# Optimization experiments

Hardware: AMD Instinct MI355X
Metric: run time of the kernel (lower is better)

## Reference

```python
import jax, jax.numpy as jnp
import numpy as np


def setup_inputs() -> dict:
    key = jax.random.key(0)
    k1, k2, k3, k4 = jax.random.split(key, 4)
    batch, n_channels, t = 4, 2048, 2048
    n_blocks, block_size, ks = 128, 64, 16
    n_block_row = n_channels // block_size  # 32
    x = jax.random.normal(k1, (batch, n_channels, t), dtype=jnp.float32)
    block_values = jax.random.normal(k2, (n_blocks, block_size, block_size, ks), dtype=jnp.float32) * 0.05
    cols = jax.random.randint(k3, (n_blocks,), 0, n_block_row, dtype=jnp.int32)
    rows = jax.random.randint(k4, (n_blocks,), 0, n_block_row, dtype=jnp.int32)
    return {"x": x, "block_values": block_values, "cols": cols, "rows": rows}


def reference(x, block_values, cols, rows):
    # x: (B, C, T); block_values: (n_blocks, bs, bs, ks)
    batch, n_channels, t = x.shape
    n_blocks, bs, _, ks = block_values.shape
    n_block_row = -(-n_channels // bs)
    pad = n_block_row * bs - n_channels
    if pad > 0:
        x = jnp.pad(x, ((0, 0), (0, pad), (0, 0)))
    xb = x.reshape(batch, n_block_row, bs, t)
    # gather active block rows: (B, n_blocks, bs, T) -> (B, n_blocks*bs, T)
    x_unfold = xb[:, cols].reshape(batch, n_blocks * bs, t)
    # grouped causal conv: weights shared across batch, groups = n_blocks
    W = block_values.reshape(n_blocks * bs, bs, ks)  # (O, I/g, K)
    o = jax.lax.conv_general_dilated(
        x_unfold, W,
        window_strides=(1,),
        padding=[(ks - 1, 0)],  # causal: equals padding=ks-1 then [..., :t]
        dimension_numbers=("NCH", "OIH", "NCH"),
        feature_group_count=n_blocks,
    )  # (B, n_blocks*bs, T)
    o = o.reshape(batch, n_blocks, bs, t)
    # scatter-add block outputs into their target block rows
    y = jnp.zeros((batch, n_block_row, bs, t), o.dtype).at[:, rows].add(o)
    y = y.reshape(batch, n_block_row * bs, t)
    return y[:, :n_channels, :]
```

## Files before the change

### kernel.cpp

```cpp
#include <hip/hip_runtime.h>
#include <hip/hip_bf16.h>
#include <stdint.h>

typedef __bf16 bf16_t;
typedef bf16_t bf16x8 __attribute__((ext_vector_type(8)));
typedef float f32x4 __attribute__((ext_vector_type(4)));

#define T_LEN 2048
#define C_LEN 2048
#define NB 128
#define TN 256
#define SROWS 2064
#define XROWS 288

#define GLL(gp, lp) __builtin_amdgcn_global_load_lds( \
    (const __attribute__((address_space(1))) uint32_t*)(gp), \
    (__attribute__((address_space(3))) uint32_t*)(lp), 16, 0, 0)

__global__ __launch_bounds__(256) void prepack_kernel(
    const float* __restrict__ bv, bf16_t* __restrict__ wpk)
{
  const int blk = blockIdx.x;
  const int mt  = blockIdx.y;
  const int tid = threadIdx.x;
  __shared__ float lw[16 * 64 * 17];

  const float* src = bv + (size_t)blk * 65536 + (size_t)mt * 16384;
  for (int p = 0; p < 16; ++p) {
    int idx = p * 1024 + tid * 4;
    const float4 v = *(const float4*)(src + idx);
    int o = idx >> 10;
    int i = (idx >> 4) & 63;
    int k = idx & 15;
    float* d = &lw[(o * 64 + i) * 17 + k];
    d[0] = v.x; d[1] = v.y; d[2] = v.z; d[3] = v.w;
  }
  __syncthreads();

  const int e0 = tid * 2;
  const int l  = e0 >> 3;
  const int j  = e0 & 7;
  const int o  = l & 15;
  for (int ks = 0; ks < 32; ++ks) {
    const int k  = ks >> 1;
    const int i0 = (ks & 1) * 32 + (l >> 4) * 8 + j;
    const float a = lw[(o * 64 + i0) * 17 + k];
    const float b = lw[(o * 64 + i0 + 1) * 17 + k];
    const uint16_t ba = __builtin_bit_cast(uint16_t, (bf16_t)a);
    const uint16_t bb = __builtin_bit_cast(uint16_t, (bf16_t)b);
    const uint32_t packed = (uint32_t)ba | ((uint32_t)bb << 16);
    const size_t off = ((((size_t)blk * 32 + ks) * 4 + mt) * 512) + e0;
    *(uint32_t*)(wpk + off) = packed;
  }
}

__global__ __launch_bounds__(256) void padzero_kernel(bf16_t* __restrict__ S)
{
  const int p = blockIdx.x;
  const size_t g = (p < 64) ? ((size_t)(p >> 4) * SROWS + (p & 15))
                            : ((size_t)4 * SROWS + (p - 64));
  uint4 z = {0u, 0u, 0u, 0u};
  *(uint4*)(S + g * C_LEN + (size_t)threadIdx.x * 8) = z;
}

__global__ __launch_bounds__(256) void xprep_kernel(
    const float* __restrict__ x, bf16_t* __restrict__ S)
{
  const int tb = blockIdx.x, cb = blockIdx.y, n = blockIdx.z;
  const int tid = threadIdx.x;
  __shared__ float lt[64 * 67 + 4];

  #pragma unroll
  for (int p = 0; p < 4; ++p) {
    const int idx = p * 256 + tid;
    const int c   = idx >> 4;
    const int t4  = (idx & 15) * 4;
    const float4 v = *(const float4*)(
        x + ((size_t)n * C_LEN + cb * 64 + c) * T_LEN + tb * 64 + t4);
    float* d = &lt[c * 67 + t4];
    d[0] = v.x; d[1] = v.y; d[2] = v.z; d[3] = v.w;
  }
  __syncthreads();

  #pragma unroll
  for (int p = 0; p < 2; ++p) {
    const int idx = p * 256 + tid;
    const int tl  = idx >> 3;
    const int seg = idx & 7;
    const int t   = tb * 64 + tl;
    const int cbase = (seg * 8) ^ ((t & 7) << 3);
    uint32_t w[4];
    #pragma unroll
    for (int h = 0; h < 4; ++h) {
      const float a = lt[(cbase + 2 * h) * 67 + tl];
      const float b = lt[(cbase + 2 * h + 1) * 67 + tl];
      const uint16_t ba = __builtin_bit_cast(uint16_t, (bf16_t)a);
      const uint16_t bb = __builtin_bit_cast(uint16_t, (bf16_t)b);
      w[h] = (uint32_t)ba | ((uint32_t)bb << 16);
    }
    uint4 u4 = {w[0], w[1], w[2], w[3]};
    *(uint4*)(S + ((size_t)n * SROWS + 16 + t) * C_LEN + cb * 64 + seg * 8) = u4;
  }
}

__global__ __launch_bounds__(256, 2) void bsconv_kernel(
    const bf16_t* __restrict__ S, const bf16_t* __restrict__ wpk,
    const int* __restrict__ cols, const int* __restrict__ rows,
    float* __restrict__ y)
{
  const int tt = blockIdx.x, tr = blockIdx.y, n = blockIdx.z;
  const int t0 = tt * TN;
  const int tid = threadIdx.x;
  const int lane = tid & 63, wv = tid >> 6;

  __shared__ __attribute__((aligned(16))) bf16_t xst[XROWS * 64];
  __shared__ __attribute__((aligned(16))) bf16_t wring[5][4096];
  __shared__ int alist[NB];
  __shared__ unsigned long long wmask[2];

  {
    const int r  = (tid < NB) ? rows[tid] : -1;
    const int cb = (tid < NB) ? cols[tid] : 0;
    const bool match = (r == tr);
    const unsigned long long m = __ballot(match);
    if (wv < 2 && lane == 0) wmask[wv] = m;
    __syncthreads();
    if (match) {
      int pos = __popcll(wmask[wv] & ((1ull << lane) - 1ull));
      if (wv == 1) pos += __popcll(wmask[0]);
      alist[pos] = tid | (cb << 8);
    }
    __syncthreads();
  }
  const int cnt = __popcll(wmask[0]) + __popcll(wmask[1]);

  f32x4 acc[4][4];
  #pragma unroll
  for (int a = 0; a < 4; ++a)
    #pragma unroll
    for (int b = 0; b < 4; ++b) {
      f32x4 z = {0.f, 0.f, 0.f, 0.f};
      acc[a][b] = z;
    }

  const size_t srow0 = (size_t)n * SROWS + t0;
  const int lxb = tid * 16;

  auto issue_x = [&](int cb) {
    #pragma unroll
    for (int q = 0; q < 9; ++q) {
      const int lb = q * 4096 + lxb;
      const int u  = lb >> 7;
      const int ib = (lb >> 1) & 63;
      GLL(S + (srow0 + u) * C_LEN + cb * 64 + ib, (char*)xst + lb);
    }
  };
  auto issue_wc = [&](const bf16_t* wblk, int c, int slot) {
    const bf16_t* wsrc = wblk + (size_t)c * 4096;
    #pragma unroll
    for (int p = 0; p < 2; ++p) {
      const int lb = p * 4096 + lxb;
      GLL(wsrc + (lb >> 1), (char*)wring[slot] + lb);
    }
  };

  bf16x8 afr[2][4], bfr[2][4];
  auto read_frags = [&](int c) {
    const bf16_t* wl = wring[c % 5];
    #pragma unroll
    for (int kk = 0; kk < 2; ++kk) {
      #pragma unroll
      for (int mt = 0; mt < 4; ++mt)
        afr[kk][mt] = *(const bf16x8*)(wl + ((kk * 4 + mt) * 64 + lane) * 8);
      const int ub   = wv * 64 + (lane & 15) + c + 1;
      const int scol = (kk * 32 + ((lane >> 4) & 3) * 8) ^ ((ub & 7) << 3);
      #pragma unroll
      for (int nt = 0; nt < 4; ++nt)
        bfr[kk][nt] = *(const bf16x8*)(xst + (ub + nt * 16) * 64 + scol);
    }
  };

  for (int j = 0; j < cnt; ++j) {
    const int aj = alist[j];
    const bf16_t* wblk = wpk + (size_t)(aj & 255) * 65536;
    const int cb = aj >> 8;

    issue_x(cb);
    issue_wc(wblk, 0, 0);
    issue_wc(wblk, 1, 1);
    issue_wc(wblk, 2, 2);
    issue_wc(wblk, 3, 3);
    asm volatile("s_waitcnt vmcnt(4)" ::: "memory");
    __builtin_amdgcn_s_barrier();
    read_frags(0);

    for (int c = 0; c < 16; ++c) {
      asm volatile("s_waitcnt lgkmcnt(0)" ::: "memory");
      __builtin_amdgcn_sched_barrier(0);
      if (c <= 11) issue_wc(wblk, c + 4, (c + 4) % 5);
      __builtin_amdgcn_s_setprio(1);
      #pragma unroll
      for (int kk = 0; kk < 2; ++kk)
        #pragma unroll
        for (int mt = 0; mt < 4; ++mt)
          #pragma unroll
          for (int nt = 0; nt < 4; ++nt)
            acc[mt][nt] = __builtin_amdgcn_mfma_f32_16x16x32_bf16(
                afr[kk][mt], bfr[kk][nt], acc[mt][nt], 0, 0, 0);
      __builtin_amdgcn_s_setprio(0);
      __builtin_amdgcn_sched_barrier(0);
      if (c < 15) {
        if (c <= 11)      asm volatile("s_waitcnt vmcnt(4)" ::: "memory");
        else if (c == 12) asm volatile("s_waitcnt vmcnt(2)" ::: "memory");
        else              asm volatile("s_waitcnt vmcnt(0)" ::: "memory");
        read_frags(c + 1);
        __builtin_amdgcn_sched_barrier(0);
      }
      __builtin_amdgcn_s_barrier();
    }
  }

  const int mlo = ((lane >> 4) & 3) * 4, nn = lane & 15;
  #pragma unroll
  for (int mt = 0; mt < 4; ++mt) {
    #pragma unroll
    for (int nt = 0; nt < 4; ++nt) {
      const int t = t0 + wv * 64 + nt * 16 + nn;
      float* yp = y + ((size_t)n * C_LEN + (size_t)(tr * 64 + mt * 16 + mlo)) * T_LEN + t;
      #pragma unroll
      for (int r = 0; r < 4; ++r)
        yp[(size_t)r * T_LEN] = acc[mt][nt][r];
    }
  }
}

extern "C" void kernel_launch(void* const* d_in, const int* in_sizes, int n_in,
                              void* d_out, int out_size, void* d_ws, size_t ws_size,
                              hipStream_t stream) {
  const float* x   = (const float*)d_in[0];
  const float* bv  = (const float*)d_in[1];
  const int* cols  = (const int*)d_in[2];
  const int* rows  = (const int*)d_in[3];
  float* y = (float*)d_out;

  bf16_t* wpk = (bf16_t*)d_ws;
  bf16_t* S   = (bf16_t*)((char*)d_ws + 16777216);

  prepack_kernel<<<dim3(128, 4), dim3(256), 0, stream>>>(bv, wpk);
  padzero_kernel<<<dim3(80), dim3(256), 0, stream>>>(S);
  xprep_kernel<<<dim3(32, 32, 4), dim3(256), 0, stream>>>(x, S);
  bsconv_kernel<<<dim3(8, 32, 4), dim3(256), 0, stream>>>(S, wpk, cols, rows, y);
}
```

Measured before the change: 175.6 us.

## Double-buffer MFMA fragments and interleave next-chunk LDS reads with MFMAs

Fragment registers are now double-buffered (A/B sets), and the 16-chunk loop is fully unrolled. The LDS reads for chunk c+1 are issued inside chunk c's MFMA block, interleaved two MFMAs per read through sched_group_barrier, instead of running serially after the MFMAs. This is meant to hide LDS read latency behind matrix math. The global-load waits are shifted so that landing is ensured one iteration earlier. The cost is roughly doubled fragment register use and larger unrolled code.

```diff
diff --git a/kernel.cpp b/kernel.cpp
--- a/kernel.cpp
+++ b/kernel.cpp
@@ -164,19 +164,20 @@
     }
   };
 
-  bf16x8 afr[2][4], bfr[2][4];
-  auto read_frags = [&](int c) {
+  bf16x8 afA[2][4], bfA[2][4], afB[2][4], bfB[2][4];
+
+  auto read_frags = [&](int c, bf16x8 (&aD)[2][4], bf16x8 (&bD)[2][4]) {
     const bf16_t* wl = wring[c % 5];
     #pragma unroll
     for (int kk = 0; kk < 2; ++kk) {
       #pragma unroll
       for (int mt = 0; mt < 4; ++mt)
-        afr[kk][mt] = *(const bf16x8*)(wl + ((kk * 4 + mt) * 64 + lane) * 8);
+        aD[kk][mt] = *(const bf16x8*)(wl + ((kk * 4 + mt) * 64 + lane) * 8);
       const int ub   = wv * 64 + (lane & 15) + c + 1;
       const int scol = (kk * 32 + ((lane >> 4) & 3) * 8) ^ ((ub & 7) << 3);
       #pragma unroll
       for (int nt = 0; nt < 4; ++nt)
-        bfr[kk][nt] = *(const bf16x8*)(xst + (ub + nt * 16) * 64 + scol);
+        bD[kk][nt] = *(const bf16x8*)(xst + (ub + nt * 16) * 64 + scol);
     }
   };
 
@@ -192,30 +193,49 @@
     issue_wc(wblk, 3, 3);
     asm volatile("s_waitcnt vmcnt(4)" ::: "memory");
     __builtin_amdgcn_s_barrier();
-    read_frags(0);
-
+    read_frags(0, afA, bfA);
+
+    #pragma unroll
     for (int c = 0; c < 16; ++c) {
       asm volatile("s_waitcnt lgkmcnt(0)" ::: "memory");
       __builtin_amdgcn_sched_barrier(0);
       if (c <= 11) issue_wc(wblk, c + 4, (c + 4) % 5);
       __builtin_amdgcn_s_setprio(1);
-      #pragma unroll
-      for (int kk = 0; kk < 2; ++kk)
+
+      if ((c & 1) == 0) {
+        if (c < 15) read_frags(c + 1, afB, bfB);
         #pragma unroll
-        for (int mt = 0; mt < 4; ++mt)
+        for (int kk = 0; kk < 2; ++kk)
           #pragma unroll
-          for (int nt = 0; nt < 4; ++nt)
-            acc[mt][nt] = __builtin_amdgcn_mfma_f32_16x16x32_bf16(
-                afr[kk][mt], bfr[kk][nt], acc[mt][nt], 0, 0, 0);
+          for (int mt = 0; mt < 4; ++mt)
+            #pragma unroll
+            for (int nt = 0; nt < 4; ++nt)
+              acc[mt][nt] = __builtin_amdgcn_mfma_f32_16x16x32_bf16(
+                  afA[kk][mt], bfA[kk][nt], acc[mt][nt], 0, 0, 0);
+      } else {
+        if (c < 15) read_frags(c + 1, afA, bfA);
+        #pragma unroll
+        for (int kk = 0; kk < 2; ++kk)
+          #pragma unroll
+          for (int mt = 0; mt < 4; ++mt)
+            #pragma unroll
+            for (int nt = 0; nt < 4; ++nt)
+              acc[mt][nt] = __builtin_amdgcn_mfma_f32_16x16x32_bf16(
+                  afB[kk][mt], bfB[kk][nt], acc[mt][nt], 0, 0, 0);
+      }
+      if (c < 15) {
+        #pragma unroll
+        for (int g = 0; g < 16; ++g) {
+          __builtin_amdgcn_sched_group_barrier(0x008, 2, 0);
+          __builtin_amdgcn_sched_group_barrier(0x100, 1, 0);
+        }
+      }
+
       __builtin_amdgcn_s_setprio(0);
       __builtin_amdgcn_sched_barrier(0);
-      if (c < 15) {
-        if (c <= 11)      asm volatile("s_waitcnt vmcnt(4)" ::: "memory");
-        else if (c == 12) asm volatile("s_waitcnt vmcnt(2)" ::: "memory");
-        else              asm volatile("s_waitcnt vmcnt(0)" ::: "memory");
-        read_frags(c + 1);
-        __builtin_amdgcn_sched_barrier(0);
-      }
+      if (c <= 11)      asm volatile("s_waitcnt vmcnt(4)" ::: "memory");
+      else if (c == 12) asm volatile("s_waitcnt vmcnt(2)" ::: "memory");
+      else if (c == 13) asm volatile("s_waitcnt vmcnt(0)" ::: "memory");
       __builtin_amdgcn_s_barrier();
     }
   }
```

Result: no change. 177.5 us, median of 2 (+1.0%).

## Reuse shifted B fragments across conv taps via DPP lane shifts

Applied to the files above, without the earlier changes.

Instead of reloading all B (x) fragments from LDS for each of the 16 taps, the kernel keeps them in registers. Each tap it shifts them by one time step with DPP row_shl, pulling the boundary element from a small per-tap patch read, which cuts LDS read traffic for B. A fragments are double-buffered and the next tap's read is issued right after the MFMA block. The tap loop is fully unrolled and the vmcnt waits are rearranged. The price is more VGPR pressure and code size, plus extra DPP/VALU work interleaved with the MFMAs.

```diff
diff --git a/kernel.cpp b/kernel.cpp
--- a/kernel.cpp
+++ b/kernel.cpp
@@ -5,6 +5,7 @@
 typedef __bf16 bf16_t;
 typedef bf16_t bf16x8 __attribute__((ext_vector_type(8)));
 typedef float f32x4 __attribute__((ext_vector_type(4)));
+typedef int int4v __attribute__((ext_vector_type(4)));
 
 #define T_LEN 2048
 #define C_LEN 2048
@@ -16,6 +17,9 @@
 #define GLL(gp, lp) __builtin_amdgcn_global_load_lds( \
     (const __attribute__((address_space(1))) uint32_t*)(gp), \
     (__attribute__((address_space(3))) uint32_t*)(lp), 16, 0, 0)
+
+#define DPP_SHL1(x) __builtin_amdgcn_update_dpp(0, (x), 0x101, 0xF, 0xF, true)
+#define DPP_SHR(x, CTRL) __builtin_amdgcn_update_dpp(0, (x), (CTRL), 0xF, 0xF, true)
 
 __global__ __launch_bounds__(256) void prepack_kernel(
     const float* __restrict__ bv, bf16_t* __restrict__ wpk)
@@ -112,6 +116,8 @@
   const int t0 = tt * TN;
   const int tid = threadIdx.x;
   const int lane = tid & 63, wv = tid >> 6;
+  const int l15 = lane & 15, lg = lane >> 4;
+  const bool is15 = (l15 == 15);
 
   __shared__ __attribute__((aligned(16))) bf16_t xst[XROWS * 64];
   __shared__ __attribute__((aligned(16))) bf16_t wring[5][4096];
@@ -164,21 +170,51 @@
     }
   };
 
-  bf16x8 afr[2][4], bfr[2][4];
-  auto read_frags = [&](int c) {
+  int4v bq[2][4];
+  int4v pq[2];
+  bf16x8 afA[2][4], afB[2][4];
+
+  auto read_A = [&](int c, bf16x8 (&aD)[2][4]) {
     const bf16_t* wl = wring[c % 5];
     #pragma unroll
+    for (int kk = 0; kk < 2; ++kk)
+      #pragma unroll
+      for (int mt = 0; mt < 4; ++mt)
+        aD[kk][mt] = *(const bf16x8*)(wl + ((kk * 4 + mt) * 64 + lane) * 8);
+  };
+  auto read_binit = [&]() {
+    #pragma unroll
+    for (int kk = 0; kk < 2; ++kk)
+      #pragma unroll
+      for (int nt = 0; nt < 4; ++nt) {
+        const int ub   = wv * 64 + l15 + 1 + nt * 16;
+        const int scol = (kk * 32 + lg * 8) ^ ((ub & 7) << 3);
+        bq[kk][nt] = *(const int4v*)(xst + ub * 64 + scol);
+      }
+  };
+  auto read_patch = [&](int c) {
+    const int pl   = (l15 < 12) ? 0 : (l15 - 12);
+    const int prow = wv * 64 + c + 17 + pl * 16;
+    #pragma unroll
     for (int kk = 0; kk < 2; ++kk) {
-      #pragma unroll
-      for (int mt = 0; mt < 4; ++mt)
-        afr[kk][mt] = *(const bf16x8*)(wl + ((kk * 4 + mt) * 64 + lane) * 8);
-      const int ub   = wv * 64 + (lane & 15) + c + 1;
-      const int scol = (kk * 32 + ((lane >> 4) & 3) * 8) ^ ((ub & 7) << 3);
-      #pragma unroll
-      for (int nt = 0; nt < 4; ++nt)
-        bfr[kk][nt] = *(const bf16x8*)(xst + (ub + nt * 16) * 64 + scol);
-    }
-  };
+      const int scol = (kk * 32 + lg * 8) ^ ((prow & 7) << 3);
+      pq[kk] = *(const int4v*)(xst + prow * 64 + scol);
+    }
+  };
+
+#define BADV(KK, NT, CTRL) do {                                           \
+    _Pragma("unroll")                                                     \
+    for (int d = 0; d < 4; ++d) {                                         \
+      const int sh = DPP_SHL1(bq[KK][NT][d]);                             \
+      const int pe = DPP_SHR(pq[KK][d], CTRL);                            \
+      bq[KK][NT][d] = is15 ? pe : sh;                                     \
+    } } while (0)
+#define BADV3(KK) do {                                                    \
+    _Pragma("unroll")                                                     \
+    for (int d = 0; d < 4; ++d) {                                         \
+      const int sh = DPP_SHL1(bq[KK][3][d]);                              \
+      bq[KK][3][d] = is15 ? pq[KK][d] : sh;                               \
+    } } while (0)
 
   for (int j = 0; j < cnt; ++j) {
     const int aj = alist[j];
@@ -192,30 +228,40 @@
     issue_wc(wblk, 3, 3);
     asm volatile("s_waitcnt vmcnt(4)" ::: "memory");
     __builtin_amdgcn_s_barrier();
-    read_frags(0);
-
+    read_A(0, afA);
+    read_binit();
+
+    #pragma unroll
     for (int c = 0; c < 16; ++c) {
       asm volatile("s_waitcnt lgkmcnt(0)" ::: "memory");
       __builtin_amdgcn_sched_barrier(0);
       if (c <= 11) issue_wc(wblk, c + 4, (c + 4) % 5);
+      if (c < 15) read_patch(c);
+
       __builtin_amdgcn_s_setprio(1);
       #pragma unroll
       for (int kk = 0; kk < 2; ++kk)
         #pragma unroll
-        for (int mt = 0; mt < 4; ++mt)
+        for (int nt = 0; nt < 4; ++nt) {
+          const bf16x8 bfr = __builtin_bit_cast(bf16x8, bq[kk][nt]);
           #pragma unroll
-          for (int nt = 0; nt < 4; ++nt)
+          for (int mt = 0; mt < 4; ++mt)
             acc[mt][nt] = __builtin_amdgcn_mfma_f32_16x16x32_bf16(
-                afr[kk][mt], bfr[kk][nt], acc[mt][nt], 0, 0, 0);
+                ((c & 1) == 0) ? afA[kk][mt] : afB[kk][mt],
+                bfr, acc[mt][nt], 0, 0, 0);
+        }
       __builtin_amdgcn_s_setprio(0);
+
+      if (c < 15) {
+        if ((c & 1) == 0) read_A(c + 1, afB);
+        else              read_A(c + 1, afA);
+        BADV(0, 0, 0x113); BADV(0, 1, 0x112); BADV(0, 2, 0x111); BADV3(0);
+        BADV(1, 0, 0x113); BADV(1, 1, 0x112); BADV(1, 2, 0x111); BADV3(1);
+      }
       __builtin_amdgcn_sched_barrier(0);
-      if (c < 15) {
-        if (c <= 11)      asm volatile("s_waitcnt vmcnt(4)" ::: "memory");
-        else if (c == 12) asm volatile("s_waitcnt vmcnt(2)" ::: "memory");
-        else              asm volatile("s_waitcnt vmcnt(0)" ::: "memory");
-        read_frags(c + 1);
-        __builtin_amdgcn_sched_barrier(0);
-      }
+      if (c <= 11)      asm volatile("s_waitcnt vmcnt(4)" ::: "memory");
+      else if (c == 12) asm volatile("s_waitcnt vmcnt(2)" ::: "memory");
+      else if (c == 13) asm volatile("s_waitcnt vmcnt(0)" ::: "memory");
       __builtin_amdgcn_s_barrier();
     }
   }
```

New measurement: 196.5 us. +11.9%, slower.
